# Kernel tuning notes

Measured on AMD Instinct MI355X. Metric: run time of the kernel, lower is better.

## Reference

```python
import jax, jax.numpy as jnp
import numpy as np

CHANNELS = 256

def setup_inputs() -> dict:
    key = jax.random.key(0)
    ks = jax.random.split(key, 7)
    B, C, N = 4, CHANNELS, 4096
    scale = 1.0 / np.sqrt(C)
    x = jax.random.normal(ks[0], (B, C, N), dtype=jnp.float32)
    Wq = jax.random.normal(ks[1], (C, C), dtype=jnp.float32) * scale
    bq = jax.random.normal(ks[2], (C,), dtype=jnp.float32) * 0.01
    Wk = jax.random.normal(ks[3], (C, C), dtype=jnp.float32) * scale
    bk = jax.random.normal(ks[4], (C,), dtype=jnp.float32) * 0.01
    Wv = jax.random.normal(ks[5], (C, C), dtype=jnp.float32) * scale
    bv = jax.random.normal(ks[6], (C,), dtype=jnp.float32) * 0.01
    return {"x": x, "Wq": Wq, "bq": bq, "Wk": Wk, "bk": bk, "Wv": Wv, "bv": bv}

def reference(x, Wq, bq, Wk, bk, Wv, bv):
    # x: [B, C, N]; 1x1 Conv1d == channel-mixing matmul
    C = x.shape[1]
    Q = jnp.einsum('oc,bcn->bon', Wq, x) + bq[None, :, None]   # [B, C, N]
    K = jnp.einsum('oc,bcn->bon', Wk, x) + bk[None, :, None]   # [B, C, N]
    V = jnp.einsum('oc,bcn->bon', Wv, x) + bv[None, :, None]   # [B, C, N]
    # attn[b, i, j] = softmax_j( Q[:, i]^T K[:, j] / sqrt(C) )
    scores = jnp.einsum('bci,bcj->bij', Q, K) / jnp.sqrt(jnp.asarray(C, x.dtype))
    attn = jax.nn.softmax(scores, axis=-1)                     # [B, N, N]
    context = jnp.einsum('bij,bcj->bci', attn, V)              # [B, C, N]
    return x + context
```

## Files before the change

### kernel.cpp

```cpp
#include <hip/hip_runtime.h>
#include <stdint.h>

#define B_ 4
#define C_ 256
#define N_ 4096
#define JS 4

typedef unsigned short u16;
typedef __attribute__((ext_vector_type(4))) float f32x4;
typedef __attribute__((ext_vector_type(16))) float f32x16;
typedef __attribute__((ext_vector_type(8))) short bf16x8;
typedef __attribute__((ext_vector_type(4))) int i32x4;

__device__ __forceinline__ u16 f2bf(float f) {
    uint32_t u = __float_as_uint(f);
    u += 0x7fffu + ((u >> 16) & 1u);
    return (u16)(u >> 16);
}
__device__ __forceinline__ float bf2f(u16 v) {
    uint32_t u = ((uint32_t)v) << 16;
    return __uint_as_float(u);
}
__device__ __forceinline__ uint32_t pkbf(float a, float b) {
    uint32_t ua = __float_as_uint(a) + 0x8000u;
    uint32_t ub = __float_as_uint(b) + 0x8000u;
    return (ua >> 16) | (ub & 0xffff0000u);
}

__device__ __forceinline__ float fexp2(float x) {
#if defined(__has_builtin)
#if __has_builtin(__builtin_amdgcn_exp2f)
    return __builtin_amdgcn_exp2f(x);
#else
    return exp2f(x);
#endif
#else
    return exp2f(x);
#endif
}

#if defined(__has_builtin)
#if __has_builtin(__builtin_amdgcn_global_load_lds)
#define HAVE_GLL 1
#endif
#endif

#ifdef HAVE_GLL
__device__ __forceinline__ void g2l16(const u16* g, u16* lbase, int lane) {
    (void)lane;
    __builtin_amdgcn_global_load_lds(
        (__attribute__((address_space(1))) void*)(uintptr_t)g,
        (__attribute__((address_space(3))) void*)lbase, 16, 0, 0);
}
#else
__device__ __forceinline__ void g2l16(const u16* g, u16* lbase, int lane) {
    *(i32x4*)(lbase + lane * 8) = *(const i32x4*)g;
}
#endif

__global__ __launch_bounds__(256) void wconv_kernel(
    const float* __restrict__ Wq, const float* __restrict__ Wk,
    const float* __restrict__ Wv, u16* __restrict__ Wb) {
    int id = blockIdx.x * 256 + threadIdx.x;
    const float* src = (id < 65536) ? Wq : ((id < 131072) ? Wk : Wv);
    Wb[id] = f2bf(src[id & 65535]);
}

__global__ __launch_bounds__(256, 2) void qkv_kernel(
    const float* __restrict__ x, const u16* __restrict__ Wb,
    const float* __restrict__ bq, const float* __restrict__ bk,
    const float* __restrict__ bv,
    u16* __restrict__ Qt, u16* __restrict__ Kt, u16* __restrict__ Vt) {
    const int XTS = 264;
    __shared__ __align__(16) u16 xT[32 * XTS];

    int blk = blockIdx.x;
    int n0  = (blk & 127) << 5;
    int b   = blk >> 7;
    int tid = threadIdx.x;
    int lane = tid & 63;
    int w = tid >> 6;
    int l31 = lane & 31;
    int h = lane >> 5;

    {
        int c0 = tid >> 3;
        int nq = (tid & 7) << 2;
        const float* xb = x + ((size_t)b * C_ + c0) * N_ + n0 + nq;
        #pragma unroll
        for (int p = 0; p < 8; ++p) {
            f32x4 v = *(const f32x4*)(xb + (size_t)32 * N_ * p);
            int cc = c0 + 32 * p;
            xT[(nq + 0) * XTS + cc] = f2bf(v[0]);
            xT[(nq + 1) * XTS + cc] = f2bf(v[1]);
            xT[(nq + 2) * XTS + cc] = f2bf(v[2]);
            xT[(nq + 3) * XTS + cc] = f2bf(v[3]);
        }
    }
    __syncthreads();

    bf16x8 xf[16];
    #pragma unroll
    for (int ks = 0; ks < 16; ++ks)
        xf[ks] = *(const bf16x8*)(&xT[l31 * XTS + 16 * ks + 8 * h]);

    #pragma unroll
    for (int mat = 0; mat < 2; ++mat) {
        const u16* W = Wb + mat * 65536;
        const float* bias = mat ? bk : bq;
        u16* dst = mat ? Kt : Qt;
        f32x16 acc0, acc1;
        #pragma unroll
        for (int r = 0; r < 16; ++r) { acc0[r] = 0.f; acc1[r] = 0.f; }
        const u16* wr0 = W + (size_t)(64 * w + l31) * 256 + 8 * h;
        const u16* wr1 = W + (size_t)(64 * w + 32 + l31) * 256 + 8 * h;
        #pragma unroll
        for (int ks = 0; ks < 16; ++ks) {
            bf16x8 wf0 = *(const bf16x8*)(wr0 + 16 * ks);
            bf16x8 wf1 = *(const bf16x8*)(wr1 + 16 * ks);
            acc0 = __builtin_amdgcn_mfma_f32_32x32x16_bf16(xf[ks], wf0, acc0, 0, 0, 0);
            acc1 = __builtin_amdgcn_mfma_f32_32x32x16_bf16(xf[ks], wf1, acc1, 0, 0, 0);
        }
        #pragma unroll
        for (int ot = 0; ot < 2; ++ot) {
            const f32x16& a = ot ? acc1 : acc0;
            int o = 64 * w + 32 * ot + l31;
            float bo = bias[o];
            #pragma unroll
            for (int g = 0; g < 4; ++g)
                #pragma unroll
                for (int r = 0; r < 4; ++r) {
                    int n = 8 * g + 4 * h + r;
                    int oc = mat ? ((((o >> 3) ^ n) << 3) | (o & 7)) : o;
                    dst[((size_t)b * N_ + n0 + n) * C_ + oc] = f2bf(a[4 * g + r] + bo);
                }
        }
    }

    {
        const u16* W = Wb + 2 * 65536;
        f32x16 acc0, acc1;
        #pragma unroll
        for (int r = 0; r < 16; ++r) { acc0[r] = 0.f; acc1[r] = 0.f; }
        const u16* wr0 = W + (size_t)(64 * w + l31) * 256 + 8 * h;
        const u16* wr1 = W + (size_t)(64 * w + 32 + l31) * 256 + 8 * h;
        #pragma unroll
        for (int ks = 0; ks < 16; ++ks) {
            bf16x8 wf0 = *(const bf16x8*)(wr0 + 16 * ks);
            bf16x8 wf1 = *(const bf16x8*)(wr1 + 16 * ks);
            acc0 = __builtin_amdgcn_mfma_f32_32x32x16_bf16(wf0, xf[ks], acc0, 0, 0, 0);
            acc1 = __builtin_amdgcn_mfma_f32_32x32x16_bf16(wf1, xf[ks], acc1, 0, 0, 0);
        }
        int nj = n0 + l31;
        int tb = nj & ~63;
        int local = nj & 63;
        #pragma unroll
        for (int mt = 0; mt < 2; ++mt) {
            const f32x16& a = mt ? acc1 : acc0;
            #pragma unroll
            for (int g = 0; g < 4; ++g)
                #pragma unroll
                for (int r = 0; r < 4; ++r) {
                    int o = 64 * w + 32 * mt + 8 * g + 4 * h + r;
                    int njs = tb | ((((local >> 3) ^ (o & 7)) << 3) | (local & 7));
                    Vt[((size_t)b * C_ + o) * N_ + njs] = f2bf(a[4 * g + r] + bv[o]);
                }
        }
    }
}

__device__ __forceinline__ void stage64(const u16* Kb, const u16* Vb, int j0,
                                        u16* ksd, u16* vsd, int w, int lane) {
    const u16* kg = Kb + (size_t)(j0 + 8 * w) * C_ + lane * 8;
    u16* kdb = ksd + 8 * w * 256;
    #pragma unroll
    for (int rr = 0; rr < 4; ++rr)
        g2l16(kg + rr * 512, kdb + rr * 512, lane);
    const u16* vg = Vb + (size_t)(32 * w + (lane >> 3)) * N_ + j0 + (lane & 7) * 8;
    u16* vdb = vsd + 32 * w * 64;
    #pragma unroll
    for (int rr = 0; rr < 4; ++rr)
        g2l16(vg + (size_t)8 * rr * N_, vdb + rr * 512, lane);
}

__global__ __launch_bounds__(512, 2) void attn_kernel(
    const u16* __restrict__ Qt, const u16* __restrict__ Kt,
    const u16* __restrict__ Vt, u16* __restrict__ Op,
    float* __restrict__ lArr) {
    __shared__ __align__(16) u16 Ksh[2 * 64 * 256];
    __shared__ __align__(16) u16 Vsh[2 * 256 * 64];

    int blk = blockIdx.x;
    int it = blk & 15;
    int b  = (blk >> 4) & 3;
    int s  = blk >> 6;
    int i0 = it << 8;
    int tid = threadIdx.x;
    int lane = tid & 63;
    int w = tid >> 6;
    int l31 = lane & 31;
    int h = lane >> 5;

    bf16x8 qf[16];
    {
        const u16* qrow = Qt + ((size_t)b * N_ + i0 + 32 * w + l31) * C_ + 8 * h;
        #pragma unroll
        for (int ks = 0; ks < 16; ++ks) qf[ks] = *(const bf16x8*)(qrow + 16 * ks);
    }

    f32x16 oacc[8];
    #pragma unroll
    for (int mt = 0; mt < 8; ++mt)
        #pragma unroll
        for (int r = 0; r < 16; ++r) oacc[mt][r] = 0.f;
    float l_run = 0.f;

    const float sconst = 0.0625f * 1.44269504088896340736f;
    const u16* Kb = Kt + (size_t)b * N_ * C_;
    const u16* Vb = Vt + (size_t)b * C_ * N_;
    int jbase = s * (N_ / JS);

    stage64(Kb, Vb, jbase, Ksh, Vsh, w, lane);
    __syncthreads();

    for (int jt = 0; jt < N_ / (64 * JS); ++jt) {
        int cur = jt & 1;
        const u16* ks_ = Ksh + cur * 64 * 256;
        const u16* vs_ = Vsh + cur * 256 * 64;

        if (jt + 1 < N_ / (64 * JS))
            stage64(Kb, Vb, jbase + (jt + 1) * 64,
                    Ksh + (cur ^ 1) * 64 * 256, Vsh + (cur ^ 1) * 256 * 64, w, lane);

        f32x16 st0, st1;
        #pragma unroll
        for (int r = 0; r < 16; ++r) { st0[r] = 0.f; st1[r] = 0.f; }
        __builtin_amdgcn_s_setprio(1);
        #pragma unroll
        for (int ks = 0; ks < 16; ++ks) {
            int kc = ((2 * ks + h) ^ l31) << 3;
            bf16x8 kf0 = *(const bf16x8*)(ks_ + l31 * 256 + kc);
            bf16x8 kf1 = *(const bf16x8*)(ks_ + (32 + l31) * 256 + kc);
            st0 = __builtin_amdgcn_mfma_f32_32x32x16_bf16(kf0, qf[ks], st0, 0, 0, 0);
            st1 = __builtin_amdgcn_mfma_f32_32x32x16_bf16(kf1, qf[ks], st1, 0, 0, 0);
        }
        __builtin_amdgcn_s_setprio(0);

        float psum = 0.f;
        uint32_t pd[16];
        #pragma unroll
        for (int u = 0; u < 8; ++u) {
            const f32x16& stv = (u < 4) ? st0 : st1;
            int g = u & 3;
            #pragma unroll
            for (int d = 0; d < 2; ++d) {
                float p0 = fexp2(stv[4 * g + 2 * d + 0] * sconst);
                float p1 = fexp2(stv[4 * g + 2 * d + 1] * sconst);
                psum += p0 + p1;
                pd[u * 2 + d] = pkbf(p0, p1);
            }
        }
        psum += __shfl_xor(psum, 32);
        l_run += psum;

        bf16x8 pf[4];
        #pragma unroll
        for (int ks2 = 0; ks2 < 4; ++ks2) {
            uint32_t oA0 = pd[4 * ks2 + 0], oA1 = pd[4 * ks2 + 1];
            uint32_t oB0 = pd[4 * ks2 + 2], oB1 = pd[4 * ks2 + 3];
            uint32_t sn0 = h ? oA0 : oB0, sn1 = h ? oA1 : oB1;
            uint32_t rc0 = (uint32_t)__shfl_xor((int)sn0, 32);
            uint32_t rc1 = (uint32_t)__shfl_xor((int)sn1, 32);
            uint32_t ow0 = h ? oB0 : oA0, ow1 = h ? oB1 : oA1;
            i32x4 fr;
            fr[0] = (int)(h ? rc0 : ow0);
            fr[1] = (int)(h ? rc1 : ow1);
            fr[2] = (int)(h ? ow0 : rc0);
            fr[3] = (int)(h ? ow1 : rc1);
            pf[ks2] = *(bf16x8*)&fr;
        }

        __builtin_amdgcn_s_setprio(1);
        #pragma unroll
        for (int ks2 = 0; ks2 < 4; ++ks2) {
            int vc = ((2 * ks2 + h) ^ (l31 & 7)) << 3;
            #pragma unroll
            for (int mt = 0; mt < 8; ++mt) {
                bf16x8 vf = *(const bf16x8*)(vs_ + (32 * mt + l31) * 64 + vc);
                oacc[mt] = __builtin_amdgcn_mfma_f32_32x32x16_bf16(vf, pf[ks2], oacc[mt], 0, 0, 0);
            }
        }
        __builtin_amdgcn_s_setprio(0);
        __syncthreads();
    }

    int i = i0 + 32 * w + l31;
    u16* ob = Op + ((size_t)(s * B_ + b) * C_) * N_ + i;
    #pragma unroll
    for (int mt = 0; mt < 8; ++mt)
        #pragma unroll
        for (int g = 0; g < 4; ++g)
            #pragma unroll
            for (int r = 0; r < 4; ++r) {
                int c = 32 * mt + 8 * g + r + 4 * h;
                ob[(size_t)c * N_] = f2bf(oacc[mt][4 * g + r]);
            }
    if (h == 0) lArr[(size_t)(s * B_ + b) * N_ + i] = l_run;
}

__global__ __launch_bounds__(256) void merge_kernel(
    const float* __restrict__ x, const u16* __restrict__ Op,
    const float* __restrict__ lArr, float* __restrict__ out) {
    __shared__ float rLs[64];
    int blk = blockIdx.x;
    int cg = blk & 3;
    int ic = (blk >> 2) & 63;
    int b  = blk >> 8;
    int i0 = ic << 6;
    int tid = threadIdx.x;

    if (tid < 64) {
        float L = 0.f;
        #pragma unroll
        for (int s = 0; s < JS; ++s) L += lArr[(size_t)(s * B_ + b) * N_ + i0 + tid];
        rLs[tid] = 1.0f / L;
    }
    __syncthreads();

    int i8 = (tid & 7) << 3;
    int c  = (cg << 6) + ((tid >> 3) << 1);
    f32x4 rl0 = *(const f32x4*)&rLs[i8];
    f32x4 rl1 = *(const f32x4*)&rLs[i8 + 4];

    #pragma unroll
    for (int cc = 0; cc < 2; ++cc) {
        size_t xoff = ((size_t)b * C_ + c + cc) * N_ + i0 + i8;
        float acc[8];
        #pragma unroll
        for (int e = 0; e < 8; ++e) acc[e] = 0.f;
        #pragma unroll
        for (int s = 0; s < JS; ++s) {
            bf16x8 o = *(const bf16x8*)&Op[((size_t)(s * B_ + b) * C_ + c + cc) * N_ + i0 + i8];
            #pragma unroll
            for (int e = 0; e < 8; ++e) acc[e] += bf2f((u16)o[e]);
        }
        f32x4 xv0 = *(const f32x4*)&x[xoff];
        f32x4 xv1 = *(const f32x4*)&x[xoff + 4];
        f32x4 o0, o1;
        #pragma unroll
        for (int e = 0; e < 4; ++e) {
            o0[e] = fmaf(acc[e], rl0[e], xv0[e]);
            o1[e] = fmaf(acc[e + 4], rl1[e], xv1[e]);
        }
        *(f32x4*)&out[xoff] = o0;
        *(f32x4*)&out[xoff + 4] = o1;
    }
}

extern "C" void kernel_launch(void* const* d_in, const int* in_sizes, int n_in,
                              void* d_out, int out_size, void* d_ws, size_t ws_size,
                              hipStream_t stream) {
    const float* x  = (const float*)d_in[0];
    const float* Wq = (const float*)d_in[1];
    const float* bq = (const float*)d_in[2];
    const float* Wk = (const float*)d_in[3];
    const float* bk = (const float*)d_in[4];
    const float* Wv = (const float*)d_in[5];
    const float* bv = (const float*)d_in[6];
    float* out = (float*)d_out;

    u16* Wb = (u16*)d_ws;
    u16* Qt = Wb + 3 * 65536;
    u16* Kt = Qt + (size_t)B_ * N_ * C_;
    u16* Vt = Kt + (size_t)B_ * N_ * C_;
    u16* Op = Vt + (size_t)B_ * N_ * C_;
    float* lArr = (float*)(Op + (size_t)JS * B_ * C_ * N_);

    wconv_kernel<<<768, 256, 0, stream>>>(Wq, Wk, Wv, Wb);
    qkv_kernel<<<512, 256, 0, stream>>>(x, Wb, bq, bk, bv, Qt, Kt, Vt);
    attn_kernel<<<256, 512, 0, stream>>>(Qt, Kt, Vt, Op, lArr);
    merge_kernel<<<1024, 256, 0, stream>>>(x, Op, lArr, out);
}
```

Before: 194.9 us.

## Fuse split-K merge into attention kernel via atomic counter barrier

```diff
diff --git a/kernel.cpp b/kernel.cpp
--- a/kernel.cpp
+++ b/kernel.cpp
@@ -60,8 +60,9 @@
 
 __global__ __launch_bounds__(256) void wconv_kernel(
     const float* __restrict__ Wq, const float* __restrict__ Wk,
-    const float* __restrict__ Wv, u16* __restrict__ Wb) {
+    const float* __restrict__ Wv, u16* __restrict__ Wb, int* __restrict__ cnt) {
     int id = blockIdx.x * 256 + threadIdx.x;
+    if (id < 64) cnt[id] = 0;
     const float* src = (id < 65536) ? Wq : ((id < 131072) ? Wk : Wv);
     Wb[id] = f2bf(src[id & 65535]);
 }
@@ -186,7 +187,8 @@
 __global__ __launch_bounds__(512, 2) void attn_kernel(
     const u16* __restrict__ Qt, const u16* __restrict__ Kt,
     const u16* __restrict__ Vt, u16* __restrict__ Op,
-    float* __restrict__ lArr) {
+    float* __restrict__ lArr, const float* __restrict__ x,
+    float* __restrict__ out, int* __restrict__ cnt) {
     __shared__ __align__(16) u16 Ksh[2 * 64 * 256];
     __shared__ __align__(16) u16 Vsh[2 * 256 * 64];
 
@@ -306,54 +308,58 @@
                 ob[(size_t)c * N_] = f2bf(oacc[mt][4 * g + r]);
             }
     if (h == 0) lArr[(size_t)(s * B_ + b) * N_ + i] = l_run;
-}
-
-__global__ __launch_bounds__(256) void merge_kernel(
-    const float* __restrict__ x, const u16* __restrict__ Op,
-    const float* __restrict__ lArr, float* __restrict__ out) {
-    __shared__ float rLs[64];
-    int blk = blockIdx.x;
-    int cg = blk & 3;
-    int ic = (blk >> 2) & 63;
-    int b  = blk >> 8;
-    int i0 = ic << 6;
-    int tid = threadIdx.x;
-
-    if (tid < 64) {
-        float L = 0.f;
-        #pragma unroll
-        for (int s = 0; s < JS; ++s) L += lArr[(size_t)(s * B_ + b) * N_ + i0 + tid];
-        rLs[tid] = 1.0f / L;
+
+    __threadfence();
+    if (tid == 0) {
+        __hip_atomic_fetch_add(&cnt[b * 16 + it], 1, __ATOMIC_ACQ_REL,
+                               __HIP_MEMORY_SCOPE_AGENT);
+        while (__hip_atomic_load(&cnt[b * 16 + it], __ATOMIC_ACQUIRE,
+                                 __HIP_MEMORY_SCOPE_AGENT) < JS)
+            __builtin_amdgcn_s_sleep(8);
     }
     __syncthreads();
-
-    int i8 = (tid & 7) << 3;
-    int c  = (cg << 6) + ((tid >> 3) << 1);
-    f32x4 rl0 = *(const f32x4*)&rLs[i8];
-    f32x4 rl1 = *(const f32x4*)&rLs[i8 + 4];
-
-    #pragma unroll
-    for (int cc = 0; cc < 2; ++cc) {
-        size_t xoff = ((size_t)b * C_ + c + cc) * N_ + i0 + i8;
-        float acc[8];
-        #pragma unroll
-        for (int e = 0; e < 8; ++e) acc[e] = 0.f;
-        #pragma unroll
-        for (int s = 0; s < JS; ++s) {
-            bf16x8 o = *(const bf16x8*)&Op[((size_t)(s * B_ + b) * C_ + c + cc) * N_ + i0 + i8];
-            #pragma unroll
-            for (int e = 0; e < 8; ++e) acc[e] += bf2f((u16)o[e]);
-        }
-        f32x4 xv0 = *(const f32x4*)&x[xoff];
-        f32x4 xv1 = *(const f32x4*)&x[xoff + 4];
-        f32x4 o0, o1;
-        #pragma unroll
-        for (int e = 0; e < 4; ++e) {
-            o0[e] = fmaf(acc[e], rl0[e], xv0[e]);
-            o1[e] = fmaf(acc[e + 4], rl1[e], xv1[e]);
-        }
-        *(f32x4*)&out[xoff] = o0;
-        *(f32x4*)&out[xoff + 4] = o1;
+    __threadfence();
+
+    {
+        float* rLs = (float*)Ksh;
+        int m0 = i0 + 64 * s;
+        if (tid < 64) {
+            float L = 0.f;
+            #pragma unroll
+            for (int ss = 0; ss < JS; ++ss)
+                L += lArr[(size_t)(ss * B_ + b) * N_ + m0 + tid];
+            rLs[tid] = 1.0f / L;
+        }
+        __syncthreads();
+
+        int i8 = (tid & 7) << 3;
+        int c0m = (tid >> 3) << 2;
+        f32x4 rl0 = *(const f32x4*)&rLs[i8];
+        f32x4 rl1 = *(const f32x4*)&rLs[i8 + 4];
+
+        #pragma unroll
+        for (int cc = 0; cc < 4; ++cc) {
+            size_t xoff = ((size_t)b * C_ + c0m + cc) * N_ + m0 + i8;
+            float acc[8];
+            #pragma unroll
+            for (int e = 0; e < 8; ++e) acc[e] = 0.f;
+            #pragma unroll
+            for (int ss = 0; ss < JS; ++ss) {
+                bf16x8 o = *(const bf16x8*)&Op[((size_t)(ss * B_ + b) * C_ + c0m + cc) * N_ + m0 + i8];
+                #pragma unroll
+                for (int e = 0; e < 8; ++e) acc[e] += bf2f((u16)o[e]);
+            }
+            f32x4 xv0 = *(const f32x4*)&x[xoff];
+            f32x4 xv1 = *(const f32x4*)&x[xoff + 4];
+            f32x4 o0, o1;
+            #pragma unroll
+            for (int e = 0; e < 4; ++e) {
+                o0[e] = fmaf(acc[e], rl0[e], xv0[e]);
+                o1[e] = fmaf(acc[e + 4], rl1[e], xv1[e]);
+            }
+            *(f32x4*)&out[xoff] = o0;
+            *(f32x4*)&out[xoff + 4] = o1;
+        }
     }
 }
 
@@ -375,9 +381,9 @@
     u16* Vt = Kt + (size_t)B_ * N_ * C_;
     u16* Op = Vt + (size_t)B_ * N_ * C_;
     float* lArr = (float*)(Op + (size_t)JS * B_ * C_ * N_);
-
-    wconv_kernel<<<768, 256, 0, stream>>>(Wq, Wk, Wv, Wb);
+    int* cnt = (int*)(lArr + (size_t)JS * B_ * N_);
+
+    wconv_kernel<<<768, 256, 0, stream>>>(Wq, Wk, Wv, Wb, cnt);
     qkv_kernel<<<512, 256, 0, stream>>>(x, Wb, bq, bk, bv, Qt, Kt, Vt);
-    attn_kernel<<<256, 512, 0, stream>>>(Qt, Kt, Vt, Op, lArr);
-    merge_kernel<<<1024, 256, 0, stream>>>(x, Op, lArr, out);
-}
+    attn_kernel<<<256, 512, 0, stream>>>(Qt, Kt, Vt, Op, lArr, x, out, cnt);
+}
```

After: 305.8 us. 1.57x slower.
